# Optimization experiments

Hardware: AMD Instinct MI355X
Metric: run time of the kernel (lower is better)

## Reference

```python
import jax, jax.numpy as jnp
import numpy as np

B, L, D, HD = 4, 4096, 2048, 128

def setup_inputs() -> dict:
    key = jax.random.key(0)
    ks = jax.random.split(key, 9)
    s = 0.02  # keep logits in a sane range
    return {
        "x": jax.random.normal(ks[0], (B, L, D), jnp.float32),
        "Wq": jax.random.normal(ks[1], (D, HD), jnp.float32) * s,
        "bq": jax.random.normal(ks[2], (HD,), jnp.float32) * s,
        "Wk": jax.random.normal(ks[3], (D, HD), jnp.float32) * s,
        "bk": jax.random.normal(ks[4], (HD,), jnp.float32) * s,
        "Wv": jax.random.normal(ks[5], (D, HD), jnp.float32) * s,
        "bv": jax.random.normal(ks[6], (HD,), jnp.float32) * s,
        "Wo": jax.random.normal(ks[7], (HD, D), jnp.float32) * s,
        "bo": jax.random.normal(ks[8], (D,), jnp.float32) * s,
    }

def reference(x, Wq, bq, Wk, bk, Wv, bv, Wo, bo):
    # x: (B, L, D)
    q = x @ Wq + bq                      # (B, L, HD)
    k = x @ Wk + bk
    v = x @ Wv + bv
    hd = q.shape[-1]
    scores = jnp.einsum('bqd,bkd->bqk', q, k) / jnp.sqrt(jnp.float32(hd))
    Lq = x.shape[1]
    causal = jnp.tril(jnp.ones((Lq, Lq), dtype=bool))  # (L, L)
    scores = jnp.where(causal, scores, -jnp.inf)
    weights = jax.nn.softmax(scores, axis=-1)          # (B, L, L)
    out = jnp.einsum('bqk,bkd->bqd', weights, v)       # (B, L, HD)
    return out @ Wo + bo                               # (B, L, D)
```

## Files before the change

### kernel.cpp

```cpp
#include <hip/hip_runtime.h>

#define B_  4
#define L_  4096
#define D_  2048
#define HD_ 128
#define M_  (B_*L_)

typedef __attribute__((ext_vector_type(8))) short short8;
typedef __attribute__((ext_vector_type(4))) float f32x4;
typedef __attribute__((ext_vector_type(16))) float f32x16;
typedef __attribute__((ext_vector_type(4))) unsigned short u16x4;
typedef __attribute__((ext_vector_type(4))) unsigned int u32x4;
typedef unsigned short u16;

#define GLL16(g, l) __builtin_amdgcn_global_load_lds( \
    (const __attribute__((address_space(1))) void*)(g), \
    (__attribute__((address_space(3))) void*)(l), 16, 0, 0)

__device__ __forceinline__ u16 f2bf(float f){
  union { float f; unsigned u; } v; v.f = f;
  unsigned r = v.u + 0x7FFFu + ((v.u >> 16) & 1u);
  return (u16)(r >> 16);
}

__device__ __forceinline__ unsigned cvtpk_bf16(float a, float b){
  unsigned r;
  asm volatile("v_cvt_pk_bf16_f32 %0, %1, %2" : "=v"(r) : "v"(a), "v"(b));
  return r;
}

__global__ __launch_bounds__(256) void prep_kernel(
    const float* __restrict__ Wq, const float* __restrict__ Wk,
    const float* __restrict__ Wv, const float* __restrict__ Wo,
    u16* __restrict__ Wt_qkv, u16* __restrict__ Wt_o)
{
  __shared__ float T[64][68];
  const int tid = threadIdx.x;
  int tb = blockIdx.x;
  int mat = tb >> 6, t = tb & 63;
  const float* src; u16* dst; int Rw, Cw, rt, ct;
  if (mat < 3) {
    src = (mat==0) ? Wq : (mat==1) ? Wk : Wv;
    dst = Wt_qkv + (size_t)mat*HD_*D_;
    Rw = D_; Cw = HD_; rt = t >> 1; ct = t & 1;
  } else {
    src = Wo; dst = Wt_o;
    Rw = HD_; Cw = D_; rt = t >> 5; ct = t & 31;
  }
  int r0 = rt*64, c0 = ct*64;
  #pragma unroll
  for (int i=0;i<4;i++){
    int fid = i*256 + tid;
    int row = fid >> 4, c4 = (fid & 15) * 4;
    float4 v = *reinterpret_cast<const float4*>(src + (size_t)(r0+row)*Cw + c0 + c4);
    *reinterpret_cast<float4*>(&T[row][c4]) = v;
  }
  __syncthreads();
  #pragma unroll
  for (int i=0;i<2;i++){
    int sid = i*256 + tid;
    int crow = sid >> 3, k8 = (sid & 7) * 8;
    short8 o;
    #pragma unroll
    for (int j=0;j<8;j++) o[j] = (short)f2bf(T[k8+j][crow]);
    *reinterpret_cast<short8*>(dst + (size_t)(c0+crow)*Rw + r0 + k8) = o;
  }
}

__global__ __launch_bounds__(512, 2) void qkv_kernel(
    const float* __restrict__ x, const u16* __restrict__ Wt,
    const float* __restrict__ bq, const float* __restrict__ bk,
    const float* __restrict__ bv,
    u16* __restrict__ Q, u16* __restrict__ K, u16* __restrict__ Vt)
{
  const int rb = blockIdx.x;
  const int tid  = threadIdx.x;
  const int lane = tid & 63, w = tid >> 6;
  const int wr = w >> 2, wc = w & 3;
  const int l15 = lane & 15, lhi = lane >> 4;
  const int row0 = rb * 64;

  __shared__ u16 Asm[64*64];
  __shared__ u16 Bsm[384*64];

  const u16* bSrc[6]; u16* bDst[6];
  #pragma unroll
  for (int i=0;i<6;i++){
    int id = i*512 + w*64 + lane;
    int r = id >> 3, c = (id & 7) * 8;
    bSrc[i] = Wt + (size_t)r*D_ + (c ^ ((r&7)*8));
    bDst[i] = Bsm + i*4096 + w*512;
  }
  const int ar = tid >> 3, ac = (tid & 7) * 8;
  const int aoff = ar*64 + (ac ^ ((ar&7)*8));
  const float* xrow = x + (size_t)(row0+ar)*D_ + ac;

  int offA[2][2], offB[2][6];
  #pragma unroll
  for (int ks=0;ks<2;ks++){
    #pragma unroll
    for (int m=0;m<2;m++){
      int rA = wr*32 + m*16 + l15;
      offA[ks][m] = rA*64 + ((ks*32 + lhi*8) ^ ((rA&7)*8));
    }
    #pragma unroll
    for (int n=0;n<6;n++){
      int rB = wc*96 + n*16 + l15;
      offB[ks][n] = rB*64 + ((ks*32 + lhi*8) ^ ((rB&7)*8));
    }
  }

  f32x4 acc[2][6];
  f32x4 zero4 = {0.f,0.f,0.f,0.f};
  #pragma unroll
  for (int m=0;m<2;m++)
    #pragma unroll
    for (int n=0;n<6;n++) acc[m][n] = zero4;

  float4 f0 = *reinterpret_cast<const float4*>(xrow);
  float4 f1 = *reinterpret_cast<const float4*>(xrow + 4);

  for (int k0 = 0; k0 < D_; k0 += 64) {
    __syncthreads();
    {
      short8 a8;
      a8[0]=(short)f2bf(f0.x); a8[1]=(short)f2bf(f0.y);
      a8[2]=(short)f2bf(f0.z); a8[3]=(short)f2bf(f0.w);
      a8[4]=(short)f2bf(f1.x); a8[5]=(short)f2bf(f1.y);
      a8[6]=(short)f2bf(f1.z); a8[7]=(short)f2bf(f1.w);
      *reinterpret_cast<short8*>(Asm + aoff) = a8;
    }
    #pragma unroll
    for (int i=0;i<6;i++){ GLL16(bSrc[i], bDst[i]); bSrc[i] += 64; }
    __syncthreads();
    if (k0 + 64 < D_) {
      const float* xp = xrow + k0 + 64;
      f0 = *reinterpret_cast<const float4*>(xp);
      f1 = *reinterpret_cast<const float4*>(xp + 4);
    }
    #pragma unroll
    for (int ks=0;ks<2;ks++){
      short8 fa[2], fb[6];
      #pragma unroll
      for (int m=0;m<2;m++) fa[m] = *reinterpret_cast<const short8*>(Asm + offA[ks][m]);
      #pragma unroll
      for (int n=0;n<6;n++) fb[n] = *reinterpret_cast<const short8*>(Bsm + offB[ks][n]);
      #pragma unroll
      for (int m=0;m<2;m++)
        #pragma unroll
        for (int n=0;n<6;n++)
          acc[m][n] = __builtin_amdgcn_mfma_f32_16x16x32_bf16(fa[m], fb[n], acc[m][n], 0, 0, 0);
    }
  }

  const float qscale = 0.08838834764831845f;
  #pragma unroll
  for (int n=0;n<6;n++){
    int col = wc*96 + n*16 + l15;
    int j = col >> 7;
    int c = col & 127;
    float bi = (j==0) ? bq[c] : (j==1) ? bk[c] : bv[c];
    #pragma unroll
    for (int m=0;m<2;m++){
      int rowb = row0 + wr*32 + m*16 + (lhi<<2);
      if (j == 0) {
        #pragma unroll
        for (int r=0;r<4;r++)
          Q[(size_t)(rowb+r)*HD_ + c] = f2bf((acc[m][n][r] + bi) * qscale);
      } else if (j == 1) {
        #pragma unroll
        for (int r=0;r<4;r++)
          K[(size_t)(rowb+r)*HD_ + c] = f2bf(acc[m][n][r] + bi);
      } else {
        int bb = rowb >> 12;
        int l  = rowb & (L_-1);
        u16x4 v4;
        #pragma unroll
        for (int r=0;r<4;r++) v4[r] = f2bf(acc[m][n][r] + bi);
        *reinterpret_cast<u16x4*>(Vt + (size_t)bb*HD_*L_ + (size_t)c*L_ + l) = v4;
      }
    }
  }
}

__global__ __launch_bounds__(256, 2) void attn_kernel(
    const u16* __restrict__ Qg, const u16* __restrict__ Kg,
    const u16* __restrict__ Vtg, u16* __restrict__ AO)
{
  const int blk = blockIdx.x;
  const int xcd = blk & 7;
  const int sub = blk >> 3;
  const int b   = xcd >> 1;
  const int strip = 127 - (2*sub + (xcd & 1));
  const int q0  = strip * 32;
  const int KT  = (strip >> 1) + 1;

  const int tid = threadIdx.x, lane = tid & 63, w = tid >> 6;
  const int l31 = lane & 31;
  const int hi  = lane >> 5;

  const u16* Qb  = Qg  + (size_t)b * L_ * HD_;
  const u16* Kb  = Kg  + (size_t)b * L_ * HD_;
  const u16* Vtb = Vtg + (size_t)b * HD_ * L_;

  __shared__ __attribute__((aligned(16))) float Ol[4][32][132];
  __shared__ float Ml[4][32], Ll[4][32];

  short8 qf[8];
  #pragma unroll
  for (int ks=0; ks<8; ks++)
    qf[ks] = *reinterpret_cast<const short8*>(
        &Qb[(size_t)(q0 + l31)*HD_ + ks*16 + hi*8]);

  f32x16 O[4];
  #pragma unroll
  for (int nb=0; nb<4; nb++)
    #pragma unroll
    for (int i=0;i<16;i++) O[nb][i] = 0.f;
  float m_ = -__builtin_inff();
  float l_ = 0.f;

  for (int kt = w; kt < KT; kt += 4) {
    const u16* Kt = Kb + (size_t)kt*64*HD_;
    f32x16 s[2];
    #pragma unroll
    for (int n=0;n<2;n++)
      #pragma unroll
      for (int i=0;i<16;i++) s[n][i] = 0.f;
    __builtin_amdgcn_s_setprio(1);
    #pragma unroll
    for (int ks=0;ks<8;ks++)
      #pragma unroll
      for (int n=0;n<2;n++){
        short8 ka = *reinterpret_cast<const short8*>(
            &Kt[(size_t)(n*32 + l31)*HD_ + ks*16 + hi*8]);
        s[n] = __builtin_amdgcn_mfma_f32_32x32x16_bf16(ka, qf[ks], s[n], 0, 0, 0);
      }
    __builtin_amdgcn_s_setprio(0);

    if (kt == KT-1) {
      #pragma unroll
      for (int n=0;n<2;n++)
        #pragma unroll
        for (int reg=0;reg<16;reg++){
          int key = kt*64 + n*32 + (reg&3) + 8*(reg>>2) + 4*hi;
          if (key > q0 + l31) s[n][reg] = -__builtin_inff();
        }
    }

    float pmax = s[0][0];
    #pragma unroll
    for (int n=0;n<2;n++)
      #pragma unroll
      for (int reg=0;reg<16;reg++) pmax = fmaxf(pmax, s[n][reg]);
    pmax = fmaxf(pmax, __shfl_xor(pmax, 32, 64));

    if (!__all(pmax <= m_ + 8.f)) {
      float mnew = fmaxf(m_, pmax);
      float alpha = __expf(m_ - mnew);
      m_ = mnew;
      l_ *= alpha;
      #pragma unroll
      for (int nb=0; nb<4; nb++)
        #pragma unroll
        for (int i=0;i<16;i++) O[nb][i] *= alpha;
    }

    float rsum = 0.f;
    #pragma unroll
    for (int n=0;n<2;n++)
      #pragma unroll
      for (int reg=0;reg<16;reg++){
        float p = __expf(s[n][reg] - m_);
        s[n][reg] = p;
        rsum += p;
      }
    rsum += __shfl_xor(rsum, 32, 64);
    l_ += rsum;

    unsigned c[2][8], ox[2][8];
    #pragma unroll
    for (int n=0;n<2;n++)
      #pragma unroll
      for (int i=0;i<8;i++)
        c[n][i] = cvtpk_bf16(s[n][2*i], s[n][2*i+1]);
    #pragma unroll
    for (int n=0;n<2;n++)
      #pragma unroll
      for (int i=0;i<8;i++)
        ox[n][i] = (unsigned)__shfl_xor((int)c[n][i], 32, 64);

    short8 pb[4];
    #pragma unroll
    for (int n=0;n<2;n++)
      #pragma unroll
      for (int sB=0;sB<2;sB++){
        union { u32x4 u; short8 s8; } t;
        t.u[0] = hi ? ox[n][4*sB+2] : c[n][4*sB+0];
        t.u[1] = hi ? ox[n][4*sB+3] : c[n][4*sB+1];
        t.u[2] = hi ? c[n][4*sB+2]  : ox[n][4*sB+0];
        t.u[3] = hi ? c[n][4*sB+3]  : ox[n][4*sB+1];
        pb[2*n+sB] = t.s8;
      }

    const u16* Vk = Vtb + (size_t)kt*64 + hi*8;
    __builtin_amdgcn_s_setprio(1);
    #pragma unroll
    for (int ks=0; ks<4; ks++){
      #pragma unroll
      for (int nb=0; nb<4; nb++){
        short8 av = *reinterpret_cast<const short8*>(
            Vk + (size_t)(nb*32 + l31)*L_ + ks*16);
        O[nb] = __builtin_amdgcn_mfma_f32_32x32x16_bf16(av, pb[ks], O[nb], 0, 0, 0);
      }
    }
    __builtin_amdgcn_s_setprio(0);
  }

  if (hi == 0) { Ml[w][l31] = m_; Ll[w][l31] = l_; }
  #pragma unroll
  for (int nb=0; nb<4; nb++)
    #pragma unroll
    for (int g=0; g<4; g++){
      f32x4 v;
      v[0]=O[nb][4*g+0]; v[1]=O[nb][4*g+1]; v[2]=O[nb][4*g+2]; v[3]=O[nb][4*g+3];
      *reinterpret_cast<f32x4*>(&Ol[w][l31][nb*32 + g*8 + hi*4]) = v;
    }
  __syncthreads();

  {
    int q  = tid >> 3;
    int dc = (tid & 7) * 16;
    float mw[4], lw[4];
    float M = -__builtin_inff();
    #pragma unroll
    for (int w2=0; w2<4; w2++){ mw[w2]=Ml[w2][q]; lw[w2]=Ll[w2][q]; M = fmaxf(M, mw[w2]); }
    float den = 0.f, cw[4];
    #pragma unroll
    for (int w2=0; w2<4; w2++){ float e = __expf(mw[w2]-M); cw[w2]=e; den += lw[w2]*e; }
    float inv = 1.0f/den;
    float o[16];
    #pragma unroll
    for (int j=0;j<16;j++) o[j] = 0.f;
    #pragma unroll
    for (int w2=0; w2<4; w2++){
      #pragma unroll
      for (int g=0; g<4; g++){
        f32x4 p = *reinterpret_cast<const f32x4*>(&Ol[w2][q][dc + g*4]);
        #pragma unroll
        for (int j=0;j<4;j++) o[g*4+j] += cw[w2]*p[j];
      }
    }
    short8 st0, st1;
    #pragma unroll
    for (int j=0;j<8;j++){ st0[j] = (short)f2bf(o[j]*inv); st1[j] = (short)f2bf(o[8+j]*inv); }
    u16* dst = &AO[((size_t)b*L_ + q0 + q)*HD_ + dc];
    *reinterpret_cast<short8*>(dst)     = st0;
    *reinterpret_cast<short8*>(dst + 8) = st1;
  }
}

__global__ __launch_bounds__(256) void proj_kernel(
    const u16* __restrict__ AO, const u16* __restrict__ Wt_o,
    const float* __restrict__ bo, float* __restrict__ out)
{
  const int nb = blockIdx.x;
  const int rb = blockIdx.y;
  const int tid = threadIdx.x, lane = tid & 63, w = tid >> 6;
  const int wr = w >> 1, wc = w & 1;
  const int l15 = lane & 15, lhi = lane >> 4;
  const int row0 = rb * 128, n0 = nb * 128;

  __shared__ u16 Al[128][136];
  __shared__ u16 Bl[128][136];

  #pragma unroll
  for (int i=0;i<8;i++){
    int chunk = i*256 + tid;
    int r = chunk >> 4;
    int c = (chunk & 15) * 8;
    *reinterpret_cast<short8*>(&Al[r][c]) =
        *reinterpret_cast<const short8*>(&AO[(size_t)(row0+r)*HD_ + c]);
    *reinterpret_cast<short8*>(&Bl[r][c]) =
        *reinterpret_cast<const short8*>(&Wt_o[(size_t)(n0+r)*HD_ + c]);
  }
  __syncthreads();

  f32x4 acc[4][4];
  f32x4 zero4 = {0.f,0.f,0.f,0.f};
  for (int m=0;m<4;m++) for (int n=0;n<4;n++) acc[m][n] = zero4;

  #pragma unroll
  for (int ks=0; ks<128; ks+=32){
    short8 fa[4], fb[4];
    #pragma unroll
    for (int m=0;m<4;m++)
      fa[m] = *reinterpret_cast<const short8*>(&Al[wr*64 + m*16 + l15][ks + (lhi<<3)]);
    #pragma unroll
    for (int n=0;n<4;n++)
      fb[n] = *reinterpret_cast<const short8*>(&Bl[wc*64 + n*16 + l15][ks + (lhi<<3)]);
    #pragma unroll
    for (int m=0;m<4;m++)
      #pragma unroll
      for (int n=0;n<4;n++)
        acc[m][n] = __builtin_amdgcn_mfma_f32_16x16x32_bf16(fa[m], fb[n], acc[m][n], 0, 0, 0);
  }

  #pragma unroll
  for (int n=0;n<4;n++){
    int col = n0 + wc*64 + n*16 + l15;
    float b = bo[col];
    #pragma unroll
    for (int m=0;m<4;m++){
      #pragma unroll
      for (int r=0;r<4;r++){
        int row = row0 + wr*64 + m*16 + (lhi<<2) + r;
        out[(size_t)row*D_ + col] = acc[m][n][r] + b;
      }
    }
  }
}

extern "C" void kernel_launch(void* const* d_in, const int* in_sizes, int n_in,
                              void* d_out, int out_size, void* d_ws, size_t ws_size,
                              hipStream_t stream) {
  const float* x  = (const float*)d_in[0];
  const float* Wq = (const float*)d_in[1];
  const float* bq = (const float*)d_in[2];
  const float* Wk = (const float*)d_in[3];
  const float* bk = (const float*)d_in[4];
  const float* Wv = (const float*)d_in[5];
  const float* bv = (const float*)d_in[6];
  const float* Wo = (const float*)d_in[7];
  const float* bo = (const float*)d_in[8];
  float* out = (float*)d_out;

  u16* ws      = (u16*)d_ws;
  u16* Wt_qkv  = ws;
  u16* Wt_o    = Wt_qkv + 3*HD_*D_;
  u16* Q       = Wt_o   + (size_t)D_*HD_;
  u16* K       = Q + (size_t)M_*HD_;
  u16* Vt      = K + (size_t)M_*HD_;
  u16* AO      = Vt + (size_t)M_*HD_;

  prep_kernel<<<256, 256, 0, stream>>>(Wq, Wk, Wv, Wo, Wt_qkv, Wt_o);
  qkv_kernel<<<256, 512, 0, stream>>>(x, Wt_qkv, bq, bk, bv, Q, K, Vt);
  attn_kernel<<<512, 256, 0, stream>>>(Q, K, Vt, AO);
  proj_kernel<<<dim3(16, 128), 256, 0, stream>>>(AO, Wt_o, bo, out);
}
```

Before: 190.5 us.

## Store K and V in MFMA-fragment order so attention loads are contiguous

The QKV kernel now writes K and V into a tiled layout that matches the per-lane operand order of the 32x32x16 MFMA, in 64-key blocks of 8192 elements. The attention kernel then reads each fragment as one contiguous 16-byte-per-lane load, so a wavefront covers 1 KB with no gaps. Previously these reads were row-strided gathers from the K and transposed-V layouts. The cost moves to scattered 2-byte and 8-byte stores in the QKV epilogue, and the producer and consumer are now coupled to this exact fragment layout.

```diff
diff --git a/kernel.cpp b/kernel.cpp
--- a/kernel.cpp
+++ b/kernel.cpp
@@ -71,7 +71,7 @@
     const float* __restrict__ x, const u16* __restrict__ Wt,
     const float* __restrict__ bq, const float* __restrict__ bk,
     const float* __restrict__ bv,
-    u16* __restrict__ Q, u16* __restrict__ K, u16* __restrict__ Vt)
+    u16* __restrict__ Q, u16* __restrict__ Kf, u16* __restrict__ Vf)
 {
   const int rb = blockIdx.x;
   const int tid  = threadIdx.x;
@@ -163,29 +163,39 @@
     #pragma unroll
     for (int m=0;m<2;m++){
       int rowb = row0 + wr*32 + m*16 + (lhi<<2);
+      int bb = rowb >> 12;
+      int l0 = rowb & (L_-1);
       if (j == 0) {
         #pragma unroll
         for (int r=0;r<4;r++)
           Q[(size_t)(rowb+r)*HD_ + c] = f2bf((acc[m][n][r] + bi) * qscale);
       } else if (j == 1) {
-        #pragma unroll
-        for (int r=0;r<4;r++)
-          K[(size_t)(rowb+r)*HD_ + c] = f2bf(acc[m][n][r] + bi);
+        int ksd = c >> 4, hid = (c >> 3) & 1, jd = c & 7;
+        #pragma unroll
+        for (int r=0;r<4;r++){
+          int l = l0 + r;
+          int kt = l >> 6, k6 = l & 63;
+          int n2 = k6 >> 5, l31k = k6 & 31;
+          Kf[((size_t)bb*64 + kt)*8192 + (n2*8 + ksd)*512 + (hid*32 + l31k)*8 + jd]
+              = f2bf(acc[m][n][r] + bi);
+        }
       } else {
-        int bb = rowb >> 12;
-        int l  = rowb & (L_-1);
+        int nbv = (c >> 5) & 3, l31v = c & 31;
+        int kt = l0 >> 6, k6 = l0 & 63;
+        int ksv = k6 >> 4, hiv = (k6 >> 3) & 1, j0 = k6 & 7;
         u16x4 v4;
         #pragma unroll
         for (int r=0;r<4;r++) v4[r] = f2bf(acc[m][n][r] + bi);
-        *reinterpret_cast<u16x4*>(Vt + (size_t)bb*HD_*L_ + (size_t)c*L_ + l) = v4;
+        *reinterpret_cast<u16x4*>(
+            Vf + ((size_t)bb*64 + kt)*8192 + (ksv*4 + nbv)*512 + (hiv*32 + l31v)*8 + j0) = v4;
       }
     }
   }
 }
 
 __global__ __launch_bounds__(256, 2) void attn_kernel(
-    const u16* __restrict__ Qg, const u16* __restrict__ Kg,
-    const u16* __restrict__ Vtg, u16* __restrict__ AO)
+    const u16* __restrict__ Qg, const u16* __restrict__ Kfg,
+    const u16* __restrict__ Vfg, u16* __restrict__ AO)
 {
   const int blk = blockIdx.x;
   const int xcd = blk & 7;
@@ -200,8 +210,8 @@
   const int hi  = lane >> 5;
 
   const u16* Qb  = Qg  + (size_t)b * L_ * HD_;
-  const u16* Kb  = Kg  + (size_t)b * L_ * HD_;
-  const u16* Vtb = Vtg + (size_t)b * HD_ * L_;
+  const u16* Kfb = Kfg + (size_t)b * 64 * 8192 + lane*8;
+  const u16* Vfb = Vfg + (size_t)b * 64 * 8192 + lane*8;
 
   __shared__ __attribute__((aligned(16))) float Ol[4][32][132];
   __shared__ float Ml[4][32], Ll[4][32];
@@ -221,7 +231,7 @@
   float l_ = 0.f;
 
   for (int kt = w; kt < KT; kt += 4) {
-    const u16* Kt = Kb + (size_t)kt*64*HD_;
+    const u16* Kt = Kfb + (size_t)kt*8192;
     f32x16 s[2];
     #pragma unroll
     for (int n=0;n<2;n++)
@@ -232,8 +242,7 @@
     for (int ks=0;ks<8;ks++)
       #pragma unroll
       for (int n=0;n<2;n++){
-        short8 ka = *reinterpret_cast<const short8*>(
-            &Kt[(size_t)(n*32 + l31)*HD_ + ks*16 + hi*8]);
+        short8 ka = *reinterpret_cast<const short8*>(Kt + (n*8 + ks)*512);
         s[n] = __builtin_amdgcn_mfma_f32_32x32x16_bf16(ka, qf[ks], s[n], 0, 0, 0);
       }
     __builtin_amdgcn_s_setprio(0);
@@ -303,14 +312,13 @@
         pb[2*n+sB] = t.s8;
       }
 
-    const u16* Vk = Vtb + (size_t)kt*64 + hi*8;
+    const u16* Vt2 = Vfb + (size_t)kt*8192;
     __builtin_amdgcn_s_setprio(1);
     #pragma unroll
     for (int ks=0; ks<4; ks++){
       #pragma unroll
       for (int nb=0; nb<4; nb++){
-        short8 av = *reinterpret_cast<const short8*>(
-            Vk + (size_t)(nb*32 + l31)*L_ + ks*16);
+        short8 av = *reinterpret_cast<const short8*>(Vt2 + (ks*4 + nb)*512);
         O[nb] = __builtin_amdgcn_mfma_f32_32x32x16_bf16(av, pb[ks], O[nb], 0, 0, 0);
       }
     }
@@ -439,12 +447,12 @@
   u16* Wt_qkv  = ws;
   u16* Wt_o    = Wt_qkv + 3*HD_*D_;
   u16* Q       = Wt_o   + (size_t)D_*HD_;
-  u16* K       = Q + (size_t)M_*HD_;
-  u16* Vt      = K + (size_t)M_*HD_;
-  u16* AO      = Vt + (size_t)M_*HD_;
+  u16* Kf      = Q + (size_t)M_*HD_;
+  u16* Vf      = Kf + (size_t)M_*HD_;
+  u16* AO      = Vf + (size_t)M_*HD_;
 
   prep_kernel<<<256, 256, 0, stream>>>(Wq, Wk, Wv, Wo, Wt_qkv, Wt_o);
-  qkv_kernel<<<256, 512, 0, stream>>>(x, Wt_qkv, bq, bk, bv, Q, K, Vt);
-  attn_kernel<<<512, 256, 0, stream>>>(Q, K, Vt, AO);
+  qkv_kernel<<<256, 512, 0, stream>>>(x, Wt_qkv, bq, bk, bv, Q, Kf, Vf);
+  attn_kernel<<<512, 256, 0, stream>>>(Q, Kf, Vf, AO);
   proj_kernel<<<dim3(16, 128), 256, 0, stream>>>(AO, Wt_o, bo, out);
 }
```

Measured after the change: 169.1 us. -11.3%, faster.
